# Kernel optimization log

Hardware: AMD Instinct MI355X
Metric: run time of the kernel (lower is better)

The kernel has to match this reference:

```python
import jax, jax.numpy as jnp
import numpy as np

N_NODES = 100000
N_EDGES = 1600000
N_GRAPHS = 128
F_IN = 4
H = 128
OUT = 2


def setup_inputs() -> dict:
    key = jax.random.key(0)
    ks = jax.random.split(key, 32)
    inp = {}
    inp["node_attr"] = jax.random.normal(ks[0], (N_NODES, F_IN), dtype=jnp.float32)
    inp["edge_index"] = jax.random.randint(ks[1], (2, N_EDGES), 0, N_NODES, dtype=jnp.int64)
    inp["batch"] = jnp.sort(jax.random.randint(ks[2], (N_NODES,), 0, N_GRAPHS, dtype=jnp.int64))
    # GraphConv params: lin_rel (weight+bias) applied to aggregated msgs, lin_root (no bias)
    dims = [(F_IN, H), (H, H), (H, H), (H, H)]
    for i, (din, dout) in enumerate(dims):
        s = 1.0 / np.sqrt(din)
        inp[f"Wr{i}"] = jax.random.uniform(ks[3 + 3 * i], (din, dout), jnp.float32, -s, s)
        inp[f"br{i}"] = jax.random.uniform(ks[4 + 3 * i], (dout,), jnp.float32, -s, s)
        inp[f"Wo{i}"] = jax.random.uniform(ks[5 + 3 * i], (din, dout), jnp.float32, -s, s)
    s = 1.0 / np.sqrt(H)
    for j, name in enumerate(["5", "6", "7", "8"]):
        inp[f"W{name}"] = jax.random.uniform(ks[16 + 2 * j], (H, H), jnp.float32, -s, s)
        inp[f"b{name}"] = jax.random.uniform(ks[17 + 2 * j], (H,), jnp.float32, -s, s)
    inp["Wl"] = jax.random.uniform(ks[30], (H, OUT), jnp.float32, -s, s)
    inp["bl"] = jax.random.uniform(ks[31], (OUT,), jnp.float32, -s, s)
    return inp


def _graph_conv(x, src, dst, Wr, br, Wo):
    # PyG GraphConv (aggr='add'): out = lin_rel(sum_{j->i} x_j) + lin_root(x_i)
    agg = jax.ops.segment_sum(x[src], dst, num_segments=N_NODES)
    return agg @ Wr + br + x @ Wo


def reference(node_attr, edge_index, batch,
              Wr0, br0, Wo0, Wr1, br1, Wo1, Wr2, br2, Wo2, Wr3, br3, Wo3,
              W5, b5, W6, b6, W7, b7, W8, b8, Wl, bl):
    src, dst = edge_index[0], edge_index[1]
    x = node_attr
    for Wr, br, Wo in [(Wr0, br0, Wo0), (Wr1, br1, Wo1), (Wr2, br2, Wo2), (Wr3, br3, Wo3)]:
        x = jax.nn.relu(_graph_conv(x, src, dst, Wr, br, Wo))
    # global mean pool over graphs
    sums = jax.ops.segment_sum(x, batch, num_segments=N_GRAPHS)
    cnt = jax.ops.segment_sum(jnp.ones((N_NODES,), x.dtype), batch, num_segments=N_GRAPHS)
    g = sums / jnp.maximum(cnt, 1.0)[:, None]
    # dropout p=0.5 is identity in eval mode
    g = jax.nn.relu(g @ W5 + b5)
    g = jax.nn.relu(g @ W6 + b6)
    g = jax.nn.relu(g @ W7 + b7)
    g = jax.nn.relu(g @ W8 + b8)
    return jax.nn.sigmoid(g @ Wl + bl)
```

## Files before the change

### kernel.cpp

```cpp
#include <hip/hip_runtime.h>
#include <hip/hip_bf16.h>
#include <math.h>

#define NN 100000
#define NE 1600000
#define NG 128
#define H 128
#define DMAX 64
#define NB 391
#define BCAP 5120
#define EPB 3125

typedef __attribute__((ext_vector_type(8))) short short8;
typedef __attribute__((ext_vector_type(4))) float floatx4;
typedef __attribute__((ext_vector_type(2))) float floatx2;
typedef __attribute__((ext_vector_type(4))) int intx4;
typedef __attribute__((ext_vector_type(4))) unsigned uintx4;

__global__ void k_init_wcvt(int* __restrict__ gbase, float* __restrict__ gsum,
                            unsigned* __restrict__ rowA, unsigned* __restrict__ rowB,
                            unsigned* __restrict__ rowF8,
                            const float* __restrict__ Wr1, const float* __restrict__ Wo1,
                            const float* __restrict__ Wr2, const float* __restrict__ Wo2,
                            const float* __restrict__ Wr3, const float* __restrict__ Wo3,
                            __hip_bfloat16* __restrict__ wf) {
  if (blockIdx.x < 384) {
    int t = blockIdx.x * 256 + threadIdx.x;
    int L = t >> 15, tt = t & 32767;
    const float* Wr = (L == 0) ? Wr1 : (L == 1) ? Wr2 : Wr3;
    const float* Wo = (L == 0) ? Wo1 : (L == 1) ? Wo2 : Wo3;
    int j = tt & 7, lanex = (tt >> 3) & 63, ct = (tt >> 9) & 7, kt = tt >> 12;
    int lr = lanex & 15, quad = lanex >> 4;
    int n = ct * 16 + lr;
    int r = kt * 32 + quad * 8 + j;
    float v = (r < 128) ? Wr[r * 128 + n] : Wo[(r - 128) * 128 + n];
    wf[t] = __float2bfloat16(v);
  } else {
    int t = (blockIdx.x - 384) * 256 + threadIdx.x;
    if (t < NB) gbase[t] = 0;
    else if (t < NB + NG * H) gsum[t - NB] = 0.f;
    else if (t < NB + NG * H + 64) rowA[t - NB - NG * H] = 0u;
    else if (t < NB + NG * H + 128) rowB[t - NB - NG * H - 64] = 0u;
    else if (t < NB + NG * H + 160) rowF8[t - NB - NG * H - 128] = 0u;
  }
}

__global__ __launch_bounds__(256) void k_bucket(const int* __restrict__ ei,
                                                int* __restrict__ gbase,
                                                int2* __restrict__ pairs) {
  __shared__ int scnt[512];
  __shared__ int soff[NB];
  __shared__ int sbase[NB];
  __shared__ int2 stg[EPB];
  __shared__ short sbkt[EPB];
  const int tid = threadIdx.x;
  const int e0 = blockIdx.x * EPB;
  const int* dst = ei + NE;

  scnt[tid] = 0;
  scnt[tid + 256] = 0;
  __syncthreads();
  for (int e = e0 + tid; e < e0 + EPB; e += 256) {
    int d = __builtin_nontemporal_load(dst + e);
    atomicAdd(&scnt[d >> 8], 1);
  }
  __syncthreads();
  int c0 = scnt[tid], c1 = scnt[tid + 256];
  for (int off = 1; off < 512; off <<= 1) {
    int v0 = (tid >= off) ? scnt[tid - off] : 0;
    int v1 = (tid + 256 >= off) ? scnt[tid + 256 - off] : 0;
    __syncthreads();
    scnt[tid] += v0;
    scnt[tid + 256] += v1;
    __syncthreads();
  }
  if (tid < NB) {
    soff[tid] = scnt[tid] - c0;
    sbase[tid] = c0 ? atomicAdd(&gbase[tid], c0) : 0;
  }
  if (tid + 256 < NB) {
    soff[tid + 256] = scnt[tid + 256] - c1;
    sbase[tid + 256] = c1 ? atomicAdd(&gbase[tid + 256], c1) : 0;
  }
  __syncthreads();
  scnt[tid] = 0;
  scnt[tid + 256] = 0;
  __syncthreads();
  for (int e = e0 + tid; e < e0 + EPB; e += 256) {
    int d = __builtin_nontemporal_load(dst + e);
    int s = __builtin_nontemporal_load(ei + e);
    int b = d >> 8;
    int p = soff[b] + atomicAdd(&scnt[b], 1);
    stg[p] = make_int2(s, d);
    sbkt[p] = (short)b;
  }
  __syncthreads();
  for (int i = tid; i < EPB; i += 256) {
    int b = sbkt[i];
    int gpos = sbase[b] + (i - soff[b]);
    if (gpos < BCAP) pairs[(size_t)b * BCAP + gpos] = stg[i];
  }
}

__global__ __launch_bounds__(256) void k_fill2(const int2* __restrict__ pairs,
                                               const int* __restrict__ gbase,
                                               int* __restrict__ fcnt,
                                               int* __restrict__ colp) {
  __shared__ int scnt[256];
  const int b = blockIdx.x;
  const int d0 = b << 8;
  const int tid = threadIdx.x;
  scnt[tid] = 0;
  __syncthreads();
  int n = gbase[b];
  if (n > BCAP) n = BCAP;
  const int2* pp = pairs + (size_t)b * BCAP;
  for (int e = tid; e < n; e += 256) {
    int2 sd = pp[e];
    int dl = sd.y - d0;
    int pos = atomicAdd(&scnt[dl], 1);
    if (pos < DMAX) colp[((size_t)(d0 + dl) << 6) + pos] = sd.x;
  }
  __syncthreads();
  int d = d0 + tid;
  if (d < NN) {
    int c = scnt[tid];
    fcnt[d] = (c > DMAX) ? DMAX : c;
  }
}

__device__ inline unsigned pk_bf16(float a, float b) {
  unsigned ua = __float_as_uint(a), ub = __float_as_uint(b);
  ua = (ua + 0x7fffu + ((ua >> 16) & 1u)) >> 16;
  ub = (ub + 0x7fffu + ((ub >> 16) & 1u)) & 0xffff0000u;
  return ua | ub;
}

__device__ inline void accf8(float* a, uint2 u) {
  floatx2 p;
  p = __builtin_amdgcn_cvt_pk_f32_fp8((int)u.x, false); a[0] += p.x; a[1] += p.y;
  p = __builtin_amdgcn_cvt_pk_f32_fp8((int)u.x, true);  a[2] += p.x; a[3] += p.y;
  p = __builtin_amdgcn_cvt_pk_f32_fp8((int)u.y, false); a[4] += p.x; a[5] += p.y;
  p = __builtin_amdgcn_cvt_pk_f32_fp8((int)u.y, true);  a[6] += p.x; a[7] += p.y;
}

__device__ inline unsigned char to_fp8(float v) {
  return (unsigned char)(__builtin_amdgcn_cvt_pk_fp8_f32(v, v, 0, false) & 0xff);
}

__global__ void k_aggf8(const uint2* __restrict__ xf8, const int* __restrict__ fcnt,
                        const int* __restrict__ colp, uintx4* __restrict__ agg) {
  int w = (blockIdx.x * blockDim.x + threadIdx.x) >> 6;
  int lane = threadIdx.x & 63;
  int qr = lane >> 4, ql = lane & 15;
  int node = 4 * w + qr;
  if (node >= NN) return;
  int cnt = fcnt[node];
  cnt = (cnt + 3) & ~3;
  const int* cp = colp + (node << 6);
  float a0[8] = {0}, a1[8] = {0}, a2[8] = {0}, a3[8] = {0};
  for (int i = 0; i < cnt; i += 4) {
    intx4 ss = __builtin_nontemporal_load((const intx4*)(cp + i));
    uint2 u0 = xf8[(size_t)ss.x * 16 + ql];
    uint2 u1 = xf8[(size_t)ss.y * 16 + ql];
    uint2 u2 = xf8[(size_t)ss.z * 16 + ql];
    uint2 u3 = xf8[(size_t)ss.w * 16 + ql];
    accf8(a0, u0);
    accf8(a1, u1);
    accf8(a2, u2);
    accf8(a3, u3);
  }
  float s[8];
#pragma unroll
  for (int t = 0; t < 8; ++t) s[t] = (a0[t] + a1[t]) + (a2[t] + a3[t]);
  uintx4 o;
  o.x = pk_bf16(s[0], s[1]);
  o.y = pk_bf16(s[2], s[3]);
  o.z = pk_bf16(s[4], s[5]);
  o.w = pk_bf16(s[6], s[7]);
  __builtin_nontemporal_store(o, agg + (size_t)node * 16 + ql);
}

__global__ void k_agg4b(const float* __restrict__ x, const int* __restrict__ fcnt,
                        int* __restrict__ colp, float* __restrict__ agg4) {
  int t = blockIdx.x * blockDim.x + threadIdx.x;
  int node = t >> 2, q = t & 3;
  if (node >= NN) return;
  int cnt = fcnt[node];
  int up = (cnt + 3) & ~3;
  int pi = cnt + q;
  if (pi < up) colp[(node << 6) + pi] = NN;
  const int* cp = colp + (node << 6);
  float4 acc = make_float4(0.f, 0.f, 0.f, 0.f);
  for (int e = q; e < cnt; e += 4) {
    float4 v = ((const float4*)x)[cp[e]];
    acc.x += v.x; acc.y += v.y; acc.z += v.z; acc.w += v.w;
  }
#pragma unroll
  for (int d = 1; d < 4; d <<= 1) {
    acc.x += __shfl_xor(acc.x, d);
    acc.y += __shfl_xor(acc.y, d);
    acc.z += __shfl_xor(acc.z, d);
    acc.w += __shfl_xor(acc.w, d);
  }
  if (q == 0) ((float4*)agg4)[node] = acc;
}

__global__ __launch_bounds__(256) void k_gemm4(
    const float* __restrict__ agg4, const float* __restrict__ x4,
    const float* __restrict__ Wr, const float* __restrict__ Wo,
    const float* __restrict__ br, __hip_bfloat16* __restrict__ out,
    unsigned char* __restrict__ out8) {
  __shared__ float sWr[512], sWo[512], sbr[128];
  int tid = threadIdx.x;
  sWr[tid] = Wr[tid]; sWr[tid + 256] = Wr[tid + 256];
  sWo[tid] = Wo[tid]; sWo[tid + 256] = Wo[tid + 256];
  if (tid < 128) sbr[tid] = br[tid];
  __syncthreads();
  int node = blockIdx.x * 16 + (tid >> 4);
  int j0 = (tid & 15) * 8;
  float4 a = ((const float4*)agg4)[node];
  float4 xv = ((const float4*)x4)[node];
  float4 b0 = *(const float4*)&sbr[j0];
  float4 b1 = *(const float4*)&sbr[j0 + 4];
  float v[8] = {b0.x, b0.y, b0.z, b0.w, b1.x, b1.y, b1.z, b1.w};
#pragma unroll
  for (int k = 0; k < 4; ++k) {
    float ak = (k == 0) ? a.x : (k == 1) ? a.y : (k == 2) ? a.z : a.w;
    float xk = (k == 0) ? xv.x : (k == 1) ? xv.y : (k == 2) ? xv.z : xv.w;
    float4 wr0 = *(const float4*)&sWr[k * 128 + j0];
    float4 wr1 = *(const float4*)&sWr[k * 128 + j0 + 4];
    float4 wo0 = *(const float4*)&sWo[k * 128 + j0];
    float4 wo1 = *(const float4*)&sWo[k * 128 + j0 + 4];
    v[0] = fmaf(ak, wr0.x, fmaf(xk, wo0.x, v[0]));
    v[1] = fmaf(ak, wr0.y, fmaf(xk, wo0.y, v[1]));
    v[2] = fmaf(ak, wr0.z, fmaf(xk, wo0.z, v[2]));
    v[3] = fmaf(ak, wr0.w, fmaf(xk, wo0.w, v[3]));
    v[4] = fmaf(ak, wr1.x, fmaf(xk, wo1.x, v[4]));
    v[5] = fmaf(ak, wr1.y, fmaf(xk, wo1.y, v[5]));
    v[6] = fmaf(ak, wr1.z, fmaf(xk, wo1.z, v[6]));
    v[7] = fmaf(ak, wr1.w, fmaf(xk, wo1.w, v[7]));
  }
#pragma unroll
  for (int jj = 0; jj < 8; ++jj) v[jj] = fmaxf(v[jj], 0.f);
  uintx4 ob;
  ob.x = pk_bf16(v[0], v[1]);
  ob.y = pk_bf16(v[2], v[3]);
  ob.z = pk_bf16(v[4], v[5]);
  ob.w = pk_bf16(v[6], v[7]);
  *(uintx4*)(out + (size_t)node * H + j0) = ob;
  unsigned w8a, w8b;
  w8a = (unsigned)__builtin_amdgcn_cvt_pk_fp8_f32(v[0], v[1], 0, false);
  w8a = (unsigned)__builtin_amdgcn_cvt_pk_fp8_f32(v[2], v[3], (int)w8a, true);
  w8b = (unsigned)__builtin_amdgcn_cvt_pk_fp8_f32(v[4], v[5], 0, false);
  w8b = (unsigned)__builtin_amdgcn_cvt_pk_fp8_f32(v[6], v[7], (int)w8b, true);
  uint2 o8; o8.x = w8a; o8.y = w8b;
  *(uint2*)(out8 + (size_t)node * H + j0) = o8;
}

__global__ __launch_bounds__(256) void k_gemm_mfma(
    const __hip_bfloat16* __restrict__ A, const __hip_bfloat16* __restrict__ X,
    const __hip_bfloat16* __restrict__ Wf, const float* __restrict__ br,
    __hip_bfloat16* __restrict__ out, unsigned char* __restrict__ out8) {
  __shared__ short8 sw[4096];
  const int tid = threadIdx.x;
  const int wv = tid >> 6, lane = tid & 63;
  const int quad = lane >> 4, lr = lane & 15;
  const int mbase = blockIdx.x * 128 + wv * 32;

#pragma unroll
  for (int i = 0; i < 16; ++i)
    sw[i * 256 + tid] = ((const short8*)Wf)[i * 256 + tid];

  floatx4 acc[2][8];
#pragma unroll
  for (int rt = 0; rt < 2; ++rt)
#pragma unroll
    for (int ct = 0; ct < 8; ++ct) acc[rt][ct] = (floatx4){0.f, 0.f, 0.f, 0.f};

  int r0 = mbase + lr;      if (r0 > NN - 1) r0 = NN - 1;
  int r1 = mbase + 16 + lr; if (r1 > NN - 1) r1 = NN - 1;

  __syncthreads();

#pragma unroll
  for (int kt = 0; kt < 8; ++kt) {
    const __hip_bfloat16* base = (kt < 4) ? A : X;
    const size_t koff = (size_t)(kt & 3) * 32 + quad * 8;
    short8 a0 = __builtin_nontemporal_load((const short8*)(base + (size_t)r0 * H + koff));
    short8 a1 = __builtin_nontemporal_load((const short8*)(base + (size_t)r1 * H + koff));
#pragma unroll
    for (int ct = 0; ct < 8; ++ct) {
      short8 b = sw[kt * 512 + ct * 64 + lane];
      acc[0][ct] = __builtin_amdgcn_mfma_f32_16x16x32_bf16(b, a0, acc[0][ct], 0, 0, 0);
      acc[1][ct] = __builtin_amdgcn_mfma_f32_16x16x32_bf16(b, a1, acc[1][ct], 0, 0, 0);
    }
  }

  floatx4 bias4[8];
#pragma unroll
  for (int ct = 0; ct < 8; ++ct)
    bias4[ct] = *(const floatx4*)(br + ct * 16 + quad * 4);

#pragma unroll
  for (int rt = 0; rt < 2; ++rt) {
    int row = mbase + rt * 16 + lr;
    if (row < NN) {
#pragma unroll
      for (int ct = 0; ct < 8; ++ct) {
        float v0 = fmaxf(acc[rt][ct][0] + bias4[ct].x, 0.f);
        float v1 = fmaxf(acc[rt][ct][1] + bias4[ct].y, 0.f);
        float v2 = fmaxf(acc[rt][ct][2] + bias4[ct].z, 0.f);
        float v3 = fmaxf(acc[rt][ct][3] + bias4[ct].w, 0.f);
        uint2 ob;
        ob.x = pk_bf16(v0, v1);
        ob.y = pk_bf16(v2, v3);
        *(uint2*)(out + (size_t)row * H + ct * 16 + quad * 4) = ob;
        unsigned w8 = 0;
        w8 = (unsigned)__builtin_amdgcn_cvt_pk_fp8_f32(v0, v1, (int)w8, false);
        w8 = (unsigned)__builtin_amdgcn_cvt_pk_fp8_f32(v2, v3, (int)w8, true);
        *(unsigned*)(out8 + (size_t)row * H + ct * 16 + quad * 4) = w8;
      }
    }
  }
}

__global__ __launch_bounds__(256) void k_gemm_mfma_pool(
    const __hip_bfloat16* __restrict__ A, const __hip_bfloat16* __restrict__ X,
    const __hip_bfloat16* __restrict__ Wf, const float* __restrict__ br,
    const int* __restrict__ batch, float* __restrict__ gsum) {
  __shared__ short8 sw[4096];
  __shared__ float pool[4][2][H];
  const int tid = threadIdx.x;
  const int wv = tid >> 6, lane = tid & 63;
  const int quad = lane >> 4, lr = lane & 15;
  const int bbase = blockIdx.x * 128;
  const int mbase = bbase + wv * 32;

#pragma unroll
  for (int i = 0; i < 16; ++i)
    sw[i * 256 + tid] = ((const short8*)Wf)[i * 256 + tid];

  floatx4 acc[2][8];
#pragma unroll
  for (int rt = 0; rt < 2; ++rt)
#pragma unroll
    for (int ct = 0; ct < 8; ++ct) acc[rt][ct] = (floatx4){0.f, 0.f, 0.f, 0.f};

  int r0 = mbase + lr;      if (r0 > NN - 1) r0 = NN - 1;
  int r1 = mbase + 16 + lr; if (r1 > NN - 1) r1 = NN - 1;

  __syncthreads();

#pragma unroll
  for (int kt = 0; kt < 8; ++kt) {
    const __hip_bfloat16* base = (kt < 4) ? A : X;
    const size_t koff = (size_t)(kt & 3) * 32 + quad * 8;
    short8 a0 = __builtin_nontemporal_load((const short8*)(base + (size_t)r0 * H + koff));
    short8 a1 = __builtin_nontemporal_load((const short8*)(base + (size_t)r1 * H + koff));
#pragma unroll
    for (int ct = 0; ct < 8; ++ct) {
      short8 b = sw[kt * 512 + ct * 64 + lane];
      acc[0][ct] = __builtin_amdgcn_mfma_f32_16x16x32_bf16(a0, b, acc[0][ct], 0, 0, 0);
      acc[1][ct] = __builtin_amdgcn_mfma_f32_16x16x32_bf16(a1, b, acc[1][ct], 0, 0, 0);
    }
  }

  const int g0 = batch[bbase];
  float bias[8];
#pragma unroll
  for (int ct = 0; ct < 8; ++ct) bias[ct] = br[ct * 16 + lr];

  float ps0[8] = {0.f, 0.f, 0.f, 0.f, 0.f, 0.f, 0.f, 0.f};
  float ps1[8] = {0.f, 0.f, 0.f, 0.f, 0.f, 0.f, 0.f, 0.f};
#pragma unroll
  for (int rt = 0; rt < 2; ++rt) {
#pragma unroll
    for (int rg = 0; rg < 4; ++rg) {
      int row = mbase + rt * 16 + quad * 4 + rg;
      if (row < NN) {
        if (batch[row] == g0) {
#pragma unroll
          for (int ct = 0; ct < 8; ++ct)
            ps0[ct] += fmaxf(acc[rt][ct][rg] + bias[ct], 0.f);
        } else {
#pragma unroll
          for (int ct = 0; ct < 8; ++ct)
            ps1[ct] += fmaxf(acc[rt][ct][rg] + bias[ct], 0.f);
        }
      }
    }
  }

#pragma unroll
  for (int ct = 0; ct < 8; ++ct) {
    float a = ps0[ct];
    a += __shfl_xor(a, 16);
    a += __shfl_xor(a, 32);
    float b = ps1[ct];
    b += __shfl_xor(b, 16);
    b += __shfl_xor(b, 32);
    if (quad == 0) {
      pool[wv][0][ct * 16 + lr] = a;
      pool[wv][1][ct * 16 + lr] = b;
    }
  }
  __syncthreads();

  if (tid < H) {
    float v = pool[0][0][tid] + pool[1][0][tid] + pool[2][0][tid] + pool[3][0][tid];
    atomicAdd(&gsum[g0 * H + tid], v);
    int rlast = bbase + 127; if (rlast > NN - 1) rlast = NN - 1;
    int g1 = batch[rlast];
    if (g1 != g0) {
      float w = pool[0][1][tid] + pool[1][1][tid] + pool[2][1][tid] + pool[3][1][tid];
      atomicAdd(&gsum[g1 * H + tid], w);
    }
  }
}

__global__ void k_head2(const float* __restrict__ gsum, const int* __restrict__ batch,
                        const float* __restrict__ W5, const float* __restrict__ b5,
                        const float* __restrict__ W6, const float* __restrict__ b6,
                        const float* __restrict__ W7, const float* __restrict__ b7,
                        const float* __restrict__ W8, const float* __restrict__ b8,
                        const float* __restrict__ Wl, const float* __restrict__ bl,
                        float* __restrict__ out) {
  __shared__ float s0[128], s1[128];
  __shared__ int sb[2];
  const int g = blockIdx.x, j = threadIdx.x;
  if (j < 2) {
    int tgt = g + j, lo = 0, hi = NN;
    while (lo < hi) {
      int mid = (lo + hi) >> 1;
      if (batch[mid] < tgt) lo = mid + 1; else hi = mid;
    }
    sb[j] = lo;
  }
  __syncthreads();
  float cnt = (float)(sb[1] - sb[0]);
  s0[j] = gsum[g * 128 + j] / fmaxf(cnt, 1.f);
  __syncthreads();
  const float* Ws[4] = {W5, W6, W7, W8};
  const float* bs[4] = {b5, b6, b7, b8};
  float* cur = s0;
  float* nxt = s1;
  for (int L = 0; L < 4; ++L) {
    const float* W = Ws[L];
    float a = bs[L][j];
    for (int k = 0; k < 128; ++k) a = fmaf(cur[k], W[k * 128 + j], a);
    nxt[j] = fmaxf(a, 0.f);
    __syncthreads();
    float* t = cur; cur = nxt; nxt = t;
  }
  if (j < 2) {
    float a = bl[j];
    for (int k = 0; k < 128; ++k) a = fmaf(cur[k], Wl[k * 2 + j], a);
    out[g * 2 + j] = 1.f / (1.f + __expf(-a));
  }
}

static inline char* ws_take(char*& p, size_t bytes) {
  char* r = p;
  p += (bytes + 255) & ~(size_t)255;
  return r;
}

extern "C" void kernel_launch(void* const* d_in, const int* in_sizes, int n_in,
                              void* d_out, int out_size, void* d_ws, size_t ws_size,
                              hipStream_t stream) {
  const float* x0 = (const float*)d_in[0];
  const int* ei = (const int*)d_in[1];
  const int* batch = (const int*)d_in[2];
  const float* Wr[4] = {(const float*)d_in[3], (const float*)d_in[6],
                        (const float*)d_in[9], (const float*)d_in[12]};
  const float* brr[4] = {(const float*)d_in[4], (const float*)d_in[7],
                         (const float*)d_in[10], (const float*)d_in[13]};
  const float* Wo[4] = {(const float*)d_in[5], (const float*)d_in[8],
                        (const float*)d_in[11], (const float*)d_in[14]};
  const float* W5 = (const float*)d_in[15];
  const float* b5 = (const float*)d_in[16];
  const float* W6 = (const float*)d_in[17];
  const float* b6 = (const float*)d_in[18];
  const float* W7 = (const float*)d_in[19];
  const float* b7 = (const float*)d_in[20];
  const float* W8 = (const float*)d_in[21];
  const float* b8 = (const float*)d_in[22];
  const float* Wl = (const float*)d_in[23];
  const float* bl = (const float*)d_in[24];
  float* out = (float*)d_out;

  char* p = (char*)d_ws;
  int* fcnt = (int*)ws_take(p, (size_t)NN * 4);
  int* colp = (int*)ws_take(p, (size_t)NN * DMAX * 4);
  __hip_bfloat16* agg = (__hip_bfloat16*)ws_take(p, (size_t)NN * H * 2);
  __hip_bfloat16* bufA = (__hip_bfloat16*)ws_take(p, (size_t)(NN + 1) * H * 2);
  __hip_bfloat16* bufB = (__hip_bfloat16*)ws_take(p, (size_t)(NN + 1) * H * 2);
  unsigned char* f8 = (unsigned char*)ws_take(p, (size_t)(NN + 1) * H);
  float* agg4 = (float*)ws_take(p, (size_t)NN * 4 * 4);
  float* gsum = (float*)ws_take(p, (size_t)NG * H * 4);
  __hip_bfloat16* wfall = (__hip_bfloat16*)ws_take(p, 3 * 32768 * 2);
  int* gbase = (int*)ws_take(p, NB * 4);
  __hip_bfloat16* wf1 = wfall;
  __hip_bfloat16* wf2 = wfall + 32768;
  __hip_bfloat16* wf3 = wfall + 65536;
  int2* pairs = (int2*)agg;
  (void)ws_size; (void)in_sizes; (void)n_in; (void)out_size;

  k_init_wcvt<<<384 + (NB + NG * H + 160 + 255) / 256, 256, 0, stream>>>(
      gbase, gsum, (unsigned*)(bufA + (size_t)NN * H), (unsigned*)(bufB + (size_t)NN * H),
      (unsigned*)(f8 + (size_t)NN * H),
      Wr[1], Wo[1], Wr[2], Wo[2], Wr[3], Wo[3], wfall);
  k_bucket<<<512, 256, 0, stream>>>(ei, gbase, pairs);
  k_fill2<<<NB, 256, 0, stream>>>(pairs, gbase, fcnt, colp);

  k_agg4b<<<(NN * 4 + 255) / 256, 256, 0, stream>>>(x0, fcnt, colp, agg4);
  k_gemm4<<<NN / 16, 256, 0, stream>>>(agg4, x0, Wr[0], Wo[0], brr[0], bufA, f8);

  k_aggf8<<<6250, 256, 0, stream>>>((const uint2*)f8, fcnt, colp, (uintx4*)agg);
  k_gemm_mfma<<<782, 256, 0, stream>>>(agg, bufA, wf1, brr[1], bufB, f8);
  k_aggf8<<<6250, 256, 0, stream>>>((const uint2*)f8, fcnt, colp, (uintx4*)agg);
  k_gemm_mfma<<<782, 256, 0, stream>>>(agg, bufB, wf2, brr[2], bufA, f8);
  k_aggf8<<<6250, 256, 0, stream>>>((const uint2*)f8, fcnt, colp, (uintx4*)agg);
  k_gemm_mfma_pool<<<782, 256, 0, stream>>>(agg, bufA, wf3, brr[3], batch, gsum);

  k_head2<<<NG, 128, 0, stream>>>(gsum, batch, W5, b5, W6, b6, W7, b7, W8, b8, Wl, bl, out);
}
```

Before: 392.7 us.

## Split fp8 feature table into two 64-column planes for aggregation gathers

Stores the fp8 node features as two planes of 64 columns each instead of one 128-byte row, and the aggregation kernel now handles one plane per block (alternating by block index). This is meant to shrink the gather working set per block and improve cache hit rates for the random neighbor reads. It costs reading each node's neighbor index list twice and uses narrower 8-lane groups per node.

```diff
diff --git a/kernel.cpp b/kernel.cpp
--- a/kernel.cpp
+++ b/kernel.cpp
@@ -17,9 +17,11 @@
 typedef __attribute__((ext_vector_type(4))) int intx4;
 typedef __attribute__((ext_vector_type(4))) unsigned uintx4;
 
+#define F8PLANE ((size_t)(NN + 1) * 64)
+
 __global__ void k_init_wcvt(int* __restrict__ gbase, float* __restrict__ gsum,
                             unsigned* __restrict__ rowA, unsigned* __restrict__ rowB,
-                            unsigned* __restrict__ rowF8,
+                            unsigned* __restrict__ f8base,
                             const float* __restrict__ Wr1, const float* __restrict__ Wo1,
                             const float* __restrict__ Wr2, const float* __restrict__ Wo2,
                             const float* __restrict__ Wr3, const float* __restrict__ Wo3,
@@ -41,7 +43,11 @@
     else if (t < NB + NG * H) gsum[t - NB] = 0.f;
     else if (t < NB + NG * H + 64) rowA[t - NB - NG * H] = 0u;
     else if (t < NB + NG * H + 128) rowB[t - NB - NG * H - 64] = 0u;
-    else if (t < NB + NG * H + 160) rowF8[t - NB - NG * H - 128] = 0u;
+    else if (t < NB + NG * H + 160) {
+      int idx = t - NB - NG * H - 128;
+      int plane = idx >> 4, word = idx & 15;
+      f8base[(plane * (size_t)(NN + 1) + NN) * 16 + word] = 0u;
+    }
   }
 }
 
@@ -144,27 +150,24 @@
   p = __builtin_amdgcn_cvt_pk_f32_fp8((int)u.y, true);  a[6] += p.x; a[7] += p.y;
 }
 
-__device__ inline unsigned char to_fp8(float v) {
-  return (unsigned char)(__builtin_amdgcn_cvt_pk_fp8_f32(v, v, 0, false) & 0xff);
-}
-
-__global__ void k_aggf8(const uint2* __restrict__ xf8, const int* __restrict__ fcnt,
-                        const int* __restrict__ colp, uintx4* __restrict__ agg) {
-  int w = (blockIdx.x * blockDim.x + threadIdx.x) >> 6;
-  int lane = threadIdx.x & 63;
-  int qr = lane >> 4, ql = lane & 15;
-  int node = 4 * w + qr;
-  if (node >= NN) return;
+__global__ void k_aggf8s(const uint2* __restrict__ xf8, const int* __restrict__ fcnt,
+                         const int* __restrict__ colp, uintx4* __restrict__ agg) {
+  const int bid = blockIdx.x;
+  const int plane = bid & 1;
+  const uint2* xp = xf8 + (size_t)plane * (NN + 1) * 8;
+  const int wv = threadIdx.x >> 6, lane = threadIdx.x & 63;
+  const int qr = lane >> 3, ql = lane & 7;
+  const int node = (bid >> 1) * 32 + wv * 8 + qr;
   int cnt = fcnt[node];
   cnt = (cnt + 3) & ~3;
   const int* cp = colp + (node << 6);
   float a0[8] = {0}, a1[8] = {0}, a2[8] = {0}, a3[8] = {0};
   for (int i = 0; i < cnt; i += 4) {
     intx4 ss = __builtin_nontemporal_load((const intx4*)(cp + i));
-    uint2 u0 = xf8[(size_t)ss.x * 16 + ql];
-    uint2 u1 = xf8[(size_t)ss.y * 16 + ql];
-    uint2 u2 = xf8[(size_t)ss.z * 16 + ql];
-    uint2 u3 = xf8[(size_t)ss.w * 16 + ql];
+    uint2 u0 = xp[(size_t)ss.x * 8 + ql];
+    uint2 u1 = xp[(size_t)ss.y * 8 + ql];
+    uint2 u2 = xp[(size_t)ss.z * 8 + ql];
+    uint2 u3 = xp[(size_t)ss.w * 8 + ql];
     accf8(a0, u0);
     accf8(a1, u1);
     accf8(a2, u2);
@@ -178,7 +181,7 @@
   o.y = pk_bf16(s[2], s[3]);
   o.z = pk_bf16(s[4], s[5]);
   o.w = pk_bf16(s[6], s[7]);
-  __builtin_nontemporal_store(o, agg + (size_t)node * 16 + ql);
+  __builtin_nontemporal_store(o, agg + (size_t)node * 16 + plane * 8 + ql);
 }
 
 __global__ void k_agg4b(const float* __restrict__ x, const int* __restrict__ fcnt,
@@ -255,7 +258,7 @@
   w8b = (unsigned)__builtin_amdgcn_cvt_pk_fp8_f32(v[4], v[5], 0, false);
   w8b = (unsigned)__builtin_amdgcn_cvt_pk_fp8_f32(v[6], v[7], (int)w8b, true);
   uint2 o8; o8.x = w8a; o8.y = w8b;
-  *(uint2*)(out8 + (size_t)node * H + j0) = o8;
+  *(uint2*)(out8 + (size_t)(j0 >> 6) * F8PLANE + (size_t)node * 64 + (j0 & 63)) = o8;
 }
 
 __global__ __launch_bounds__(256) void k_gemm_mfma(
@@ -319,7 +322,8 @@
         unsigned w8 = 0;
         w8 = (unsigned)__builtin_amdgcn_cvt_pk_fp8_f32(v0, v1, (int)w8, false);
         w8 = (unsigned)__builtin_amdgcn_cvt_pk_fp8_f32(v2, v3, (int)w8, true);
-        *(unsigned*)(out8 + (size_t)row * H + ct * 16 + quad * 4) = w8;
+        *(unsigned*)(out8 + (size_t)(ct >> 2) * F8PLANE + (size_t)row * 64 +
+                     ((ct & 3) * 16 + quad * 4)) = w8;
       }
     }
   }
@@ -496,7 +500,7 @@
   __hip_bfloat16* agg = (__hip_bfloat16*)ws_take(p, (size_t)NN * H * 2);
   __hip_bfloat16* bufA = (__hip_bfloat16*)ws_take(p, (size_t)(NN + 1) * H * 2);
   __hip_bfloat16* bufB = (__hip_bfloat16*)ws_take(p, (size_t)(NN + 1) * H * 2);
-  unsigned char* f8 = (unsigned char*)ws_take(p, (size_t)(NN + 1) * H);
+  unsigned char* f8 = (unsigned char*)ws_take(p, 2 * F8PLANE);
   float* agg4 = (float*)ws_take(p, (size_t)NN * 4 * 4);
   float* gsum = (float*)ws_take(p, (size_t)NG * H * 4);
   __hip_bfloat16* wfall = (__hip_bfloat16*)ws_take(p, 3 * 32768 * 2);
@@ -509,7 +513,7 @@
 
   k_init_wcvt<<<384 + (NB + NG * H + 160 + 255) / 256, 256, 0, stream>>>(
       gbase, gsum, (unsigned*)(bufA + (size_t)NN * H), (unsigned*)(bufB + (size_t)NN * H),
-      (unsigned*)(f8 + (size_t)NN * H),
+      (unsigned*)f8,
       Wr[1], Wo[1], Wr[2], Wo[2], Wr[3], Wo[3], wfall);
   k_bucket<<<512, 256, 0, stream>>>(ei, gbase, pairs);
   k_fill2<<<NB, 256, 0, stream>>>(pairs, gbase, fcnt, colp);
@@ -517,11 +521,11 @@
   k_agg4b<<<(NN * 4 + 255) / 256, 256, 0, stream>>>(x0, fcnt, colp, agg4);
   k_gemm4<<<NN / 16, 256, 0, stream>>>(agg4, x0, Wr[0], Wo[0], brr[0], bufA, f8);
 
-  k_aggf8<<<6250, 256, 0, stream>>>((const uint2*)f8, fcnt, colp, (uintx4*)agg);
+  k_aggf8s<<<6250, 256, 0, stream>>>((const uint2*)f8, fcnt, colp, (uintx4*)agg);
   k_gemm_mfma<<<782, 256, 0, stream>>>(agg, bufA, wf1, brr[1], bufB, f8);
-  k_aggf8<<<6250, 256, 0, stream>>>((const uint2*)f8, fcnt, colp, (uintx4*)agg);
+  k_aggf8s<<<6250, 256, 0, stream>>>((const uint2*)f8, fcnt, colp, (uintx4*)agg);
   k_gemm_mfma<<<782, 256, 0, stream>>>(agg, bufB, wf2, brr[2], bufA, f8);
-  k_aggf8<<<6250, 256, 0, stream>>>((const uint2*)f8, fcnt, colp, (uintx4*)agg);
+  k_aggf8s<<<6250, 256, 0, stream>>>((const uint2*)f8, fcnt, colp, (uintx4*)agg);
   k_gemm_mfma_pool<<<782, 256, 0, stream>>>(agg, bufA, wf3, brr[3], batch, gsum);
 
   k_head2<<<NG, 128, 0, stream>>>(gsum, batch, W5, b5, W6, b6, W7, b7, W8, b8, Wl, bl, out);
```

After: 426.5 us. 8.6% more time.
